# Kernel optimization log

Hardware: AMD Instinct MI355X
Metric: run time of the kernel (lower is better)

The kernel has to match this reference:

```python
import jax, jax.numpy as jnp
import numpy as np

D = 1024      # latent_dimension
NH = 8        # num_heads
ND = 256      # drug num_functions
NT = 128      # target num_functions
B = 128       # batch
EPS_LN = 1e-5
EPS_COS = 1e-8


def _proj_attend(x, W, b, in_w, in_b, out_w, out_b, g, beta):
    """ParallelFcWithAttention.forward: per-feature Linear(1,D)+ReLU, MHSA, LN, sum.
    x: (B, >=F); W,b: (F, D); in_w: (3D, D); out_w: (D, D); g,beta: (D,)."""
    F = W.shape[0]
    # fused batched scale+bias+ReLU replacing the Python loop of Linear(1,D)
    h = jax.nn.relu(x[:, :F, None] * W[None] + b[None])           # (B, F, D)
    Bsz = h.shape[0]
    qkv = h @ in_w.T + in_b                                       # (B, F, 3D)
    q, k, v = jnp.split(qkv, 3, axis=-1)
    Dh = D // NH
    def split_heads(t):
        return t.reshape(Bsz, F, NH, Dh).transpose(0, 2, 1, 3)   # (B, H, F, Dh)
    q, k, v = split_heads(q), split_heads(k), split_heads(v)
    scale = np.float32(1.0 / np.sqrt(Dh))
    scores = jnp.einsum('bhqd,bhkd->bhqk', q, k) * scale          # (B, H, F, F)
    attn = jax.nn.softmax(scores, axis=-1)
    o = jnp.einsum('bhqk,bhkd->bhqd', attn, v)                    # (B, H, F, Dh)
    o = o.transpose(0, 2, 1, 3).reshape(Bsz, F, D)
    o = o @ out_w.T + out_b
    mu = o.mean(axis=-1, keepdims=True)
    var = ((o - mu) ** 2).mean(axis=-1, keepdims=True)
    o = (o - mu) / jnp.sqrt(var + EPS_LN) * g + beta              # LayerNorm
    return o.sum(axis=1)                                          # (B, D)


def setup_inputs() -> dict:
    key = jax.random.key(0)
    ks = jax.random.split(key, 20)
    s = np.float32(0.02)
    inp = {
        'drug':    jax.random.normal(ks[0], (B, 2048), jnp.float32),
        'target':  jax.random.normal(ks[1], (B, 1024), jnp.float32),
        'dW':      jax.random.normal(ks[2], (ND, D), jnp.float32) * s,
        'db':      jax.random.normal(ks[3], (ND, D), jnp.float32) * s,
        'd_in_w':  jax.random.normal(ks[4], (3 * D, D), jnp.float32) * s,
        'd_in_b':  jnp.zeros((3 * D,), jnp.float32),
        'd_out_w': jax.random.normal(ks[5], (D, D), jnp.float32) * s,
        'd_out_b': jnp.zeros((D,), jnp.float32),
        'd_g':     jnp.ones((D,), jnp.float32),
        'd_beta':  jnp.zeros((D,), jnp.float32),
        'tW':      jax.random.normal(ks[6], (NT, D), jnp.float32) * s,
        'tb':      jax.random.normal(ks[7], (NT, D), jnp.float32) * s,
        't_in_w':  jax.random.normal(ks[8], (3 * D, D), jnp.float32) * s,
        't_in_b':  jnp.zeros((3 * D,), jnp.float32),
        't_out_w': jax.random.normal(ks[9], (D, D), jnp.float32) * s,
        't_out_b': jnp.zeros((D,), jnp.float32),
        't_g':     jnp.ones((D,), jnp.float32),
        't_beta':  jnp.zeros((D,), jnp.float32),
    }
    return inp


def reference(drug, target, dW, db, d_in_w, d_in_b, d_out_w, d_out_b, d_g, d_beta,
              tW, tb, t_in_w, t_in_b, t_out_w, t_out_b, t_g, t_beta):
    dp = _proj_attend(drug, dW, db, d_in_w, d_in_b, d_out_w, d_out_b, d_g, d_beta)   # (B, D)
    tp = _proj_attend(target, tW, tb, t_in_w, t_in_b, t_out_w, t_out_b, t_g, t_beta) # (B, D)
    # Cosine similarity over latent dim (torch CosineSimilarity dim=1), then sigmoid
    dot = jnp.sum(dp * tp, axis=-1)
    denom = jnp.maximum(jnp.linalg.norm(dp, axis=-1) * jnp.linalg.norm(tp, axis=-1), EPS_COS)
    return jax.nn.sigmoid(dot / denom)                                               # (B,)
```

## Files before the change

### kernel.cpp

```cpp
#include <hip/hip_runtime.h>

typedef unsigned short u16;
typedef unsigned int   u32;
typedef unsigned char  u8;

using bf16x8 = __attribute__((ext_vector_type(8))) short;
using f32x4  = __attribute__((ext_vector_type(4))) float;
using i32x4  = __attribute__((ext_vector_type(4))) int;

__device__ __forceinline__ float bf2f(u16 h) {
  u32 u = ((u32)h) << 16;
  return __builtin_bit_cast(float, u);
}
__device__ __forceinline__ u16 f2bf(float f) {
  u32 u = __builtin_bit_cast(u32, f);
  u += 0x7fffu + ((u >> 16) & 1u);
  return (u16)(u >> 16);
}

__device__ __forceinline__ void gload16(const void* src, void* ldsdst) {
  __builtin_amdgcn_global_load_lds(
      (const __attribute__((address_space(1))) void*)src,
      (__attribute__((address_space(3))) void*)ldsdst, 16, 0, 0);
}

__device__ __forceinline__ void mfma_i8(i32x4& c, i32x4 a, i32x4 b) {
  asm volatile("v_mfma_i32_16x16x64_i8 %0, %1, %2, %0" : "+a"(c) : "v"(a), "v"(b));
}

__device__ __forceinline__ int xcd_swz(int wg, int nwg) {
  int q = nwg >> 3, r = nwg & 7, xcd = wg & 7, loc = wg >> 3;
  return (xcd < r ? xcd * (q + 1) : r * (q + 1) + (xcd - r) * q) + loc;
}

__global__ __launch_bounds__(256) void cvt_w_i8(const float* __restrict__ in,
                                                u8* __restrict__ out,
                                                float* __restrict__ sc) {
  const int row  = blockIdx.x * 4 + (threadIdx.x >> 6);
  const int lane = threadIdx.x & 63;
  const float4* p = (const float4*)(in + (size_t)row * 1024 + lane * 16);
  float v[16];
  float mx = 0.f;
#pragma unroll
  for (int i = 0; i < 4; ++i) {
    float4 t = p[i];
    v[i * 4 + 0] = t.x; v[i * 4 + 1] = t.y; v[i * 4 + 2] = t.z; v[i * 4 + 3] = t.w;
#pragma unroll
    for (int j = 0; j < 4; ++j) mx = fmaxf(mx, fabsf(v[i * 4 + j]));
  }
#pragma unroll
  for (int m = 1; m < 64; m <<= 1) mx = fmaxf(mx, __shfl_xor(mx, m));
  const float scale = mx > 0.f ? 127.f / mx : 0.f;
  u32 pk[4];
#pragma unroll
  for (int i = 0; i < 4; ++i) {
    u32 b0 = (u32)(__float2int_rn(v[i * 4 + 0] * scale) & 0xff);
    u32 b1 = (u32)(__float2int_rn(v[i * 4 + 1] * scale) & 0xff);
    u32 b2 = (u32)(__float2int_rn(v[i * 4 + 2] * scale) & 0xff);
    u32 b3 = (u32)(__float2int_rn(v[i * 4 + 3] * scale) & 0xff);
    pk[i] = b0 | (b1 << 8) | (b2 << 16) | (b3 << 24);
  }
  *(uint4*)(out + (size_t)row * 1024 + lane * 16) = make_uint4(pk[0], pk[1], pk[2], pk[3]);
  if (lane == 0) sc[row] = mx > 0.f ? mx / 127.f : 0.f;
}

__global__ __launch_bounds__(256) void quant_i8(const u16* __restrict__ in,
                                                u8* __restrict__ out,
                                                float* __restrict__ sc) {
  const int row  = blockIdx.x * 4 + (threadIdx.x >> 6);
  const int lane = threadIdx.x & 63;
  const u16* p = in + (size_t)row * 1024 + lane * 16;
  float v[16];
  float mx = 0.f;
#pragma unroll
  for (int i = 0; i < 2; ++i) {
    bf16x8 t = *(const bf16x8*)(p + i * 8);
#pragma unroll
    for (int j = 0; j < 8; ++j) {
      float f = bf2f((u16)t[j]);
      v[i * 8 + j] = f;
      mx = fmaxf(mx, fabsf(f));
    }
  }
#pragma unroll
  for (int m = 1; m < 64; m <<= 1) mx = fmaxf(mx, __shfl_xor(mx, m));
  const float scale = mx > 0.f ? 127.f / mx : 0.f;
  u32 pk[4];
#pragma unroll
  for (int i = 0; i < 4; ++i) {
    u32 b0 = (u32)(__float2int_rn(v[i * 4 + 0] * scale) & 0xff);
    u32 b1 = (u32)(__float2int_rn(v[i * 4 + 1] * scale) & 0xff);
    u32 b2 = (u32)(__float2int_rn(v[i * 4 + 2] * scale) & 0xff);
    u32 b3 = (u32)(__float2int_rn(v[i * 4 + 3] * scale) & 0xff);
    pk[i] = b0 | (b1 << 8) | (b2 << 16) | (b3 << 24);
  }
  *(uint4*)(out + (size_t)row * 1024 + lane * 16) = make_uint4(pk[0], pk[1], pk[2], pk[3]);
  if (lane == 0) sc[row] = mx > 0.f ? mx / 127.f : 0.f;
}

__global__ __launch_bounds__(256) void hgen_i8(const float* __restrict__ x,
                                               const float* __restrict__ W,
                                               const float* __restrict__ bias,
                                               u8* __restrict__ h, float* __restrict__ hsc,
                                               int F, int logF, int b0, int xstride) {
  const int row  = blockIdx.x * 4 + (threadIdx.x >> 6);
  const int lane = threadIdx.x & 63;
  const int f = row & (F - 1);
  const int b = b0 + (row >> logF);
  const float xv = x[(size_t)b * xstride + f];
  const float4* wp = (const float4*)(W + (size_t)f * 1024 + lane * 16);
  const float4* bp = (const float4*)(bias + (size_t)f * 1024 + lane * 16);
  float hv[16];
  float mx = 0.f;
#pragma unroll
  for (int i = 0; i < 4; ++i) {
    float4 wv = wp[i];
    float4 bv = bp[i];
    hv[i * 4 + 0] = fmaxf(xv * wv.x + bv.x, 0.f);
    hv[i * 4 + 1] = fmaxf(xv * wv.y + bv.y, 0.f);
    hv[i * 4 + 2] = fmaxf(xv * wv.z + bv.z, 0.f);
    hv[i * 4 + 3] = fmaxf(xv * wv.w + bv.w, 0.f);
#pragma unroll
    for (int j = 0; j < 4; ++j) mx = fmaxf(mx, hv[i * 4 + j]);
  }
#pragma unroll
  for (int m = 1; m < 64; m <<= 1) mx = fmaxf(mx, __shfl_xor(mx, m));
  const float scale = mx > 0.f ? 127.f / mx : 0.f;
  u32 pk[4];
#pragma unroll
  for (int i = 0; i < 4; ++i) {
    u32 q0 = (u32)__float2int_rn(hv[i * 4 + 0] * scale);
    u32 q1 = (u32)__float2int_rn(hv[i * 4 + 1] * scale);
    u32 q2 = (u32)__float2int_rn(hv[i * 4 + 2] * scale);
    u32 q3 = (u32)__float2int_rn(hv[i * 4 + 3] * scale);
    pk[i] = q0 | (q1 << 8) | (q2 << 16) | (q3 << 24);
  }
  *(uint4*)(h + (size_t)row * 1024 + lane * 16) = make_uint4(pk[0], pk[1], pk[2], pk[3]);
  if (lane == 0) hsc[row] = mx > 0.f ? mx / 127.f : 0.f;
}

__global__ __launch_bounds__(512, 4) void gemm_i8(const u8* __restrict__ A,
                                                  const u8* __restrict__ B,
                                                  const float* __restrict__ sAsc,
                                                  const float* __restrict__ sBsc,
                                                  const float* __restrict__ bias,
                                                  u16* __restrict__ C,
                                                  int M, int N, int K) {
  __shared__ u8 sA[3][256 * 64];
  __shared__ u8 sB[3][128 * 64];
  const int tid  = threadIdx.x;
  const int lane = tid & 63;
  const int w    = tid >> 6;
  const int wm   = w >> 1;
  const int wn   = w & 1;

  const int nwg = gridDim.x * gridDim.y;
  const int wg  = blockIdx.y * gridDim.x + blockIdx.x;
  const int swz = xcd_swz(wg, nwg);
  const int n0 = (swz % gridDim.x) * 128;
  const int m0 = (swz / gridDim.x) * 256;

  i32x4 acc[4][4] = {};

  const int r_in  = lane >> 2;
  const int s_src = (lane & 3) ^ ((lane >> 3) & 3);

  auto stage = [&](int kt, int b) {
    const int k0 = kt << 6;
    gload16(A + (size_t)(m0 + w * 16 + r_in) * K + k0 + s_src * 16, &sA[b][w * 1024]);
    gload16(A + (size_t)(m0 + (w + 8) * 16 + r_in) * K + k0 + s_src * 16, &sA[b][(w + 8) * 1024]);
    gload16(B + (size_t)(n0 + w * 16 + r_in) * K + k0 + s_src * 16, &sB[b][w * 1024]);
  };

  const int NT = K >> 6;
  stage(0, 0);
  stage(1, 1);
  asm volatile("s_waitcnt vmcnt(3)" ::: "memory");
  __builtin_amdgcn_s_barrier();

  int cur = 0, nx = 2;
  for (int t = 0; t < NT; ++t) {
    const bool more = (t + 2 < NT);
    if (more) stage(t + 2, nx);

    i32x4 af[4], bg[4];
    const int g = lane >> 4;
#pragma unroll
    for (int mf = 0; mf < 4; ++mf) {
      int ra = wm * 64 + mf * 16 + (lane & 15);
      af[mf] = *(const i32x4*)(&sA[cur][ra * 64 + ((g ^ ((ra >> 1) & 3)) * 16)]);
    }
#pragma unroll
    for (int nf = 0; nf < 4; ++nf) {
      int rb = wn * 64 + nf * 16 + (lane & 15);
      bg[nf] = *(const i32x4*)(&sB[cur][rb * 64 + ((g ^ ((rb >> 1) & 3)) * 16)]);
    }
    asm volatile("s_waitcnt lgkmcnt(0)" ::: "memory");
    __builtin_amdgcn_sched_barrier(0);
    __builtin_amdgcn_s_setprio(1);
#pragma unroll
    for (int mf = 0; mf < 4; ++mf)
#pragma unroll
      for (int nf = 0; nf < 4; ++nf)
        mfma_i8(acc[mf][nf], af[mf], bg[nf]);
    __builtin_amdgcn_s_setprio(0);
    if (more) asm volatile("s_waitcnt vmcnt(3)" ::: "memory");
    else      asm volatile("s_waitcnt vmcnt(0)" ::: "memory");
    __builtin_amdgcn_s_barrier();
    cur = (cur == 2) ? 0 : cur + 1;
    nx  = (nx  == 2) ? 0 : nx  + 1;
  }

#pragma unroll
  for (int nf = 0; nf < 4; ++nf) {
    int cl = n0 + wn * 64 + nf * 16 + (lane & 15);
    float sb  = sBsc[cl];
    float bsv = bias[cl];
#pragma unroll
    for (int mf = 0; mf < 4; ++mf) {
      int r0 = m0 + wm * 64 + mf * 16 + (lane >> 4) * 4;
      float4 sa4 = *(const float4*)(sAsc + r0);
      const float* sap = (const float*)&sa4;
#pragma unroll
      for (int reg = 0; reg < 4; ++reg)
        C[(size_t)(r0 + reg) * N + cl] =
            f2bf((float)acc[mf][nf][reg] * (sap[reg] * sb) + bsv);
    }
  }
}

__global__ __launch_bounds__(512, 4) void attn(const u16* __restrict__ qkv,
                                               u16* __restrict__ o_out, int F) {
  __shared__ u16 k_lds[64 * 136];
  __shared__ u16 vT[128 * 72];
  __shared__ u16 p_lds[8 * 16 * 72];

  const int tid  = threadIdx.x;
  const int lane = tid & 63;
  const int w    = tid >> 6;

  const int swzb = xcd_swz(blockIdx.x, gridDim.x);
  const int nqb  = F >> 7;
  const int qb   = swzb % nqb;
  const int head = (swzb / nqb) & 7;
  const int bc   = swzb / (nqb * 8);

  const size_t rowbase = (size_t)bc * F * 3072;
  const float scale = 0.08838834764831845f;

  const int qr = lane & 15;
  const int g4 = lane >> 4;

  bf16x8 qreg[4];
  {
    const u16* qsrc = qkv + rowbase +
                      (size_t)(qb * 128 + w * 16 + qr) * 3072 + head * 128;
#pragma unroll
    for (int kk = 0; kk < 4; ++kk) {
      bf16x8 v = *(const bf16x8*)(qsrc + kk * 32 + 8 * g4);
#pragma unroll
      for (int j = 0; j < 8; ++j) v[j] = (short)f2bf(bf2f((u16)v[j]) * scale);
      qreg[kk] = v;
    }
  }

  f32x4 o_acc[8] = {};
  float m_run = -INFINITY, l_run = 0.f;

  const int nkb = F >> 6;
  for (int kb = 0; kb < nkb; ++kb) {
    __syncthreads();
    const u16* ksrc = qkv + rowbase + (size_t)(kb * 64) * 3072 + 1024 + head * 128;
    const u16* vsrc = ksrc + 1024;
    for (int it = tid; it < 1024; it += 512) {
      int r = it >> 4, s = it & 15;
      *(bf16x8*)(k_lds + r * 136 + s * 8) = *(const bf16x8*)(ksrc + (size_t)r * 3072 + s * 8);
    }
    {
      int g2 = tid >> 4, s = tid & 15;
      const u16* v0 = vsrc + (size_t)(2 * g2) * 3072 + s * 8;
      bf16x8 a = *(const bf16x8*)(v0);
      bf16x8 b = *(const bf16x8*)(v0 + 3072);
      int rs0 = (2 * g2) ^ ((s & 7) << 3);
      int d0  = s * 8;
#pragma unroll
      for (int j = 0; j < 8; ++j) {
        u32 pk = (u32)(u16)a[j] | ((u32)(u16)b[j] << 16);
        *(u32*)(vT + (d0 + j) * 72 + rs0) = pk;
      }
    }
    __syncthreads();

    f32x4 sa[4] = {};
#pragma unroll
    for (int kk = 0; kk < 4; ++kk) {
#pragma unroll
      for (int f = 0; f < 4; ++f) {
        bf16x8 ak = *(const bf16x8*)(k_lds + (f * 16 + qr) * 136 + kk * 32 + 8 * g4);
        sa[f] = __builtin_amdgcn_mfma_f32_16x16x32_bf16(ak, qreg[kk], sa[f], 0, 0, 0);
      }
    }

    float tmax = -INFINITY;
#pragma unroll
    for (int f = 0; f < 4; ++f)
#pragma unroll
      for (int rr = 0; rr < 4; ++rr) tmax = fmaxf(tmax, sa[f][rr]);
    tmax = fmaxf(tmax, __shfl_xor(tmax, 16));
    tmax = fmaxf(tmax, __shfl_xor(tmax, 32));
    float mnew  = fmaxf(m_run, tmax);
    float alpha = __expf(m_run - mnew);
    float psum  = 0.f;
#pragma unroll
    for (int f = 0; f < 4; ++f) {
      u16 pp[4];
#pragma unroll
      for (int rr = 0; rr < 4; ++rr) {
        float p = __expf(sa[f][rr] - mnew);
        psum += p;
        pp[rr] = f2bf(p);
      }
      uint2 u;
      u.x = (u32)pp[0] | ((u32)pp[1] << 16);
      u.y = (u32)pp[2] | ((u32)pp[3] << 16);
      *(uint2*)(p_lds + w * 1152 + qr * 72 + f * 16 + g4 * 4) = u;
    }
    psum += __shfl_xor(psum, 16);
    psum += __shfl_xor(psum, 32);
    l_run = l_run * alpha + psum;
    m_run = mnew;

#pragma unroll
    for (int rr = 0; rr < 4; ++rr) {
      float ar = __shfl(alpha, g4 * 4 + rr);
#pragma unroll
      for (int g = 0; g < 8; ++g) o_acc[g][rr] *= ar;
    }

#pragma unroll
    for (int kk2 = 0; kk2 < 2; ++kk2) {
      bf16x8 pa = *(const bf16x8*)(p_lds + w * 1152 + qr * 72 + kk2 * 32 + 8 * g4);
#pragma unroll
      for (int g = 0; g < 8; ++g) {
        int swv = ((g * 2 + (qr >> 3)) & 7) << 3;
        bf16x8 vb = *(const bf16x8*)(vT + (g * 16 + qr) * 72 + ((kk2 * 32 + 8 * g4) ^ swv));
        o_acc[g] = __builtin_amdgcn_mfma_f32_16x16x32_bf16(pa, vb, o_acc[g], 0, 0, 0);
      }
    }
  }

  float linv = 1.f / l_run;
#pragma unroll
  for (int rr = 0; rr < 4; ++rr) {
    float lr = __shfl(linv, g4 * 4 + rr);
    size_t row = (size_t)bc * F + qb * 128 + w * 16 + g4 * 4 + rr;
#pragma unroll
    for (int g = 0; g < 8; ++g)
      o_out[row * 1024 + head * 128 + g * 16 + qr] = f2bf(o_acc[g][rr] * lr);
  }
}

__global__ __launch_bounds__(256) void ln_stats(const u16* __restrict__ proj,
                                                float2* __restrict__ stats) {
  int row  = blockIdx.x * 4 + (threadIdx.x >> 6);
  int lane = threadIdx.x & 63;
  const u16* p = proj + (size_t)row * 1024;
  float s = 0.f, s2 = 0.f;
#pragma unroll
  for (int i = 0; i < 2; ++i) {
    bf16x8 v = *(const bf16x8*)(p + (lane + i * 64) * 8);
#pragma unroll
    for (int j = 0; j < 8; ++j) { float f = bf2f((u16)v[j]); s += f; s2 += f * f; }
  }
#pragma unroll
  for (int m = 1; m < 64; m <<= 1) { s += __shfl_xor(s, m); s2 += __shfl_xor(s2, m); }
  if (lane == 0) {
    float mu  = s * (1.f / 1024.f);
    float var = s2 * (1.f / 1024.f) - mu * mu;
    stats[row] = make_float2(mu, rsqrtf(var + 1e-5f));
  }
}

__global__ __launch_bounds__(256) void ln_accum(const u16* __restrict__ proj,
                                                const float2* __restrict__ stats,
                                                const float* __restrict__ g,
                                                const float* __restrict__ beta,
                                                float* __restrict__ dp, int F, int b0) {
  int d  = blockIdx.x * 256 + threadIdx.x;
  int bc = blockIdx.z;
  int f0 = blockIdx.y * 64;
  const u16* base = proj + ((size_t)(bc * F + f0)) * 1024 + d;
  const float2* st = stats + bc * F + f0;
  float acc = 0.f;
  for (int f = 0; f < 64; ++f) {
    float2 s = st[f];
    acc += (bf2f(base[(size_t)f * 1024]) - s.x) * s.y;
  }
  acc = acc * g[d] + 64.f * beta[d];
  atomicAdd(&dp[(size_t)(b0 + bc) * 1024 + d], acc);
}

__global__ __launch_bounds__(256) void cosine_sig(const float* __restrict__ dp,
                                                  const float* __restrict__ tp,
                                                  float* __restrict__ out) {
  __shared__ float red[3][4];
  int b = blockIdx.x;
  int tid = threadIdx.x, lane = tid & 63, w = tid >> 6;
  float dot = 0.f, n1 = 0.f, n2 = 0.f;
  for (int i = tid; i < 1024; i += 256) {
    float a = dp[(size_t)b * 1024 + i], c = tp[(size_t)b * 1024 + i];
    dot += a * c; n1 += a * a; n2 += c * c;
  }
#pragma unroll
  for (int m = 1; m < 64; m <<= 1) {
    dot += __shfl_xor(dot, m); n1 += __shfl_xor(n1, m); n2 += __shfl_xor(n2, m);
  }
  if (lane == 0) { red[0][w] = dot; red[1][w] = n1; red[2][w] = n2; }
  __syncthreads();
  if (tid == 0) {
    dot = red[0][0] + red[0][1] + red[0][2] + red[0][3];
    n1  = red[1][0] + red[1][1] + red[1][2] + red[1][3];
    n2  = red[2][0] + red[2][1] + red[2][2] + red[2][3];
    float denom = fmaxf(sqrtf(n1) * sqrtf(n2), 1e-8f);
    out[b] = 1.f / (1.f + __expf(-dot / denom));
  }
}

extern "C" void kernel_launch(void* const* d_in, const int* in_sizes, int n_in,
                              void* d_out, int out_size, void* d_ws, size_t ws_size,
                              hipStream_t stream) {
  const float* drug   = (const float*)d_in[0];
  const float* target = (const float*)d_in[1];

  char* p = (char*)d_ws;
  auto alloc = [&](size_t bytes) -> char* {
    char* r = p; p += (bytes + 255) & ~(size_t)255; return r;
  };

  u8*    w8_d    = (u8*)alloc((size_t)3072 * 1024);
  float* wsc_d   = (float*)alloc((size_t)3072 * 4);
  u8*    w8_t    = (u8*)alloc((size_t)3072 * 1024);
  float* wsc_t   = (float*)alloc((size_t)3072 * 4);
  u8*    w8o_d   = (u8*)alloc((size_t)1024 * 1024);
  float* wsco_d  = (float*)alloc((size_t)1024 * 4);
  u8*    w8o_t   = (u8*)alloc((size_t)1024 * 1024);
  float* wsco_t  = (float*)alloc((size_t)1024 * 4);
  float* dp      = (float*)alloc((size_t)2 * 128 * 1024 * 4);
  float* tp      = dp + 128 * 1024;

  size_t fixed = (size_t)(p - (char*)d_ws);
  size_t per = (size_t)256 * 1024
             + (size_t)256 * 4
             + (size_t)256 * 3072 * 2
             + (size_t)256 * 1024 * 2 * 2
             + (size_t)256 * 8 + 4096;
  int Bc = 8;
  if      (fixed + 128 * per <= ws_size) Bc = 128;
  else if (fixed +  64 * per <= ws_size) Bc = 64;
  else if (fixed +  32 * per <= ws_size) Bc = 32;
  else if (fixed +  16 * per <= ws_size) Bc = 16;

  u8*    h8     = (u8*)alloc((size_t)Bc * 256 * 1024);
  float* hsc    = (float*)alloc((size_t)Bc * 256 * 4);
  u16*   qkvbuf = (u16*)alloc((size_t)Bc * 256 * 3072 * 2);
  u16*   obuf   = (u16*)alloc((size_t)Bc * 256 * 1024 * 2);
  u16*   projbuf= (u16*)alloc((size_t)Bc * 256 * 1024 * 2);
  float2* statsb = (float2*)alloc((size_t)Bc * 256 * 8);

  cvt_w_i8<<<768, 256, 0, stream>>>((const float*)d_in[4],  w8_d, wsc_d);
  cvt_w_i8<<<768, 256, 0, stream>>>((const float*)d_in[12], w8_t, wsc_t);
  cvt_w_i8<<<256, 256, 0, stream>>>((const float*)d_in[6],  w8o_d, wsco_d);
  cvt_w_i8<<<256, 256, 0, stream>>>((const float*)d_in[14], w8o_t, wsco_t);
  hipMemsetAsync(dp, 0, (size_t)2 * 128 * 1024 * 4, stream);

  for (int br = 0; br < 2; ++br) {
    const int F = br ? 128 : 256, logF = br ? 7 : 8, xstride = br ? 1024 : 2048;
    const float* x    = br ? target : drug;
    const float* W    = (const float*)d_in[br ? 10 : 2];
    const float* Wb   = (const float*)d_in[br ? 11 : 3];
    u8*          w8   = br ? w8_t : w8_d;
    float*       wsc  = br ? wsc_t : wsc_d;
    const float* inb  = (const float*)d_in[br ? 13 : 5];
    u8*          w8o  = br ? w8o_t : w8o_d;
    float*       wsco = br ? wsco_t : wsco_d;
    const float* outb = (const float*)d_in[br ? 15 : 7];
    const float* gg   = (const float*)d_in[br ? 16 : 8];
    const float* bb   = (const float*)d_in[br ? 17 : 9];
    float*       accp = br ? tp : dp;

    const int nb = (br ? (2 * Bc > 128 ? 128 : 2 * Bc) : (Bc > 128 ? 128 : Bc));

    for (int b0 = 0; b0 < 128; b0 += nb) {
      const int Mr = nb * F;
      hgen_i8<<<Mr / 4, 256, 0, stream>>>(x, W, Wb, h8, hsc, F, logF, b0, xstride);
      gemm_i8<<<dim3(3072 / 128, Mr / 256), 512, 0, stream>>>(h8, w8, hsc, wsc, inb, qkvbuf, Mr, 3072, 1024);
      attn<<<(F / 128) * 8 * nb, 512, 0, stream>>>(qkvbuf, obuf, F);
      quant_i8<<<Mr / 4, 256, 0, stream>>>(obuf, h8, hsc);
      gemm_i8<<<dim3(1024 / 128, Mr / 256), 512, 0, stream>>>(h8, w8o, hsc, wsco, outb, projbuf, Mr, 1024, 1024);
      ln_stats<<<Mr / 4, 256, 0, stream>>>(projbuf, statsb);
      ln_accum<<<dim3(4, F / 64, nb), 256, 0, stream>>>(projbuf, statsb, gg, bb, accp, F, b0);
    }
  }
  cosine_sig<<<128, 256, 0, stream>>>(dp, tp, (float*)d_out);
}
```

Measured before the change: 579.7 us.

## Fuse LayerNorm stats into out-proj GEMM epilogue; restructure attention block per head

The out-projection GEMM epilogue now accumulates per-row sum and sum-of-squares and adds them into a zeroed stats buffer with atomics. A tiny finalize kernel replaces the separate ln_stats pass, so the projection no longer has to be re-read. Attention now launches one block per (batch, head) with F/16 waves, so K/V tiles are loaded once per head instead of once per 128-query block. Softmax switches to exp2 with the log2e factor folded into the Q scale, and rescaling is skipped unless the max grows by more than 8. Costs are atomic contention, an extra memset, and large blocks that limit occupancy for F=256.

```diff
diff --git a/kernel.cpp b/kernel.cpp
--- a/kernel.cpp
+++ b/kernel.cpp
@@ -139,12 +139,14 @@
   if (lane == 0) hsc[row] = mx > 0.f ? mx / 127.f : 0.f;
 }
 
+template <bool STATS>
 __global__ __launch_bounds__(512, 4) void gemm_i8(const u8* __restrict__ A,
                                                   const u8* __restrict__ B,
                                                   const float* __restrict__ sAsc,
                                                   const float* __restrict__ sBsc,
                                                   const float* __restrict__ bias,
                                                   u16* __restrict__ C,
+                                                  float2* __restrict__ stats,
                                                   int M, int N, int K) {
   __shared__ u8 sA[3][256 * 64];
   __shared__ u8 sB[3][128 * 64];
@@ -211,50 +213,72 @@
     nx  = (nx  == 2) ? 0 : nx  + 1;
   }
 
+  float sb4[4], bs4[4];
 #pragma unroll
   for (int nf = 0; nf < 4; ++nf) {
     int cl = n0 + wn * 64 + nf * 16 + (lane & 15);
-    float sb  = sBsc[cl];
-    float bsv = bias[cl];
-#pragma unroll
-    for (int mf = 0; mf < 4; ++mf) {
-      int r0 = m0 + wm * 64 + mf * 16 + (lane >> 4) * 4;
-      float4 sa4 = *(const float4*)(sAsc + r0);
-      const float* sap = (const float*)&sa4;
-#pragma unroll
-      for (int reg = 0; reg < 4; ++reg)
-        C[(size_t)(r0 + reg) * N + cl] =
-            f2bf((float)acc[mf][nf][reg] * (sap[reg] * sb) + bsv);
-    }
-  }
-}
-
-__global__ __launch_bounds__(512, 4) void attn(const u16* __restrict__ qkv,
-                                               u16* __restrict__ o_out, int F) {
+    sb4[nf] = sBsc[cl];
+    bs4[nf] = bias[cl];
+  }
+#pragma unroll
+  for (int mf = 0; mf < 4; ++mf) {
+    int r0 = m0 + wm * 64 + mf * 16 + (lane >> 4) * 4;
+    float4 sa4 = *(const float4*)(sAsc + r0);
+    const float* sap = (const float*)&sa4;
+#pragma unroll
+    for (int reg = 0; reg < 4; ++reg) {
+      float s = 0.f, s2 = 0.f;
+#pragma unroll
+      for (int nf = 0; nf < 4; ++nf) {
+        int cl = n0 + wn * 64 + nf * 16 + (lane & 15);
+        float v = (float)acc[mf][nf][reg] * (sap[reg] * sb4[nf]) + bs4[nf];
+        C[(size_t)(r0 + reg) * N + cl] = f2bf(v);
+        if (STATS) { s += v; s2 += v * v; }
+      }
+      if (STATS) {
+#pragma unroll
+        for (int m = 1; m < 16; m <<= 1) { s += __shfl_xor(s, m); s2 += __shfl_xor(s2, m); }
+        if ((lane & 15) == 0) {
+          atomicAdd(&stats[r0 + reg].x, s);
+          atomicAdd(&stats[r0 + reg].y, s2);
+        }
+      }
+    }
+  }
+}
+
+__global__ __launch_bounds__(256) void ln_fin(float2* __restrict__ stats, int n) {
+  int i = blockIdx.x * 256 + threadIdx.x;
+  if (i >= n) return;
+  float2 s = stats[i];
+  float mu  = s.x * (1.f / 1024.f);
+  float var = s.y * (1.f / 1024.f) - mu * mu;
+  stats[i] = make_float2(mu, rsqrtf(var + 1e-5f));
+}
+
+__global__ __launch_bounds__(1024) void attn(const u16* __restrict__ qkv,
+                                             u16* __restrict__ o_out, int F) {
   __shared__ u16 k_lds[64 * 136];
   __shared__ u16 vT[128 * 72];
-  __shared__ u16 p_lds[8 * 16 * 72];
+  __shared__ u16 p_lds[16 * 16 * 72];
 
   const int tid  = threadIdx.x;
   const int lane = tid & 63;
   const int w    = tid >> 6;
-
-  const int swzb = xcd_swz(blockIdx.x, gridDim.x);
-  const int nqb  = F >> 7;
-  const int qb   = swzb % nqb;
-  const int head = (swzb / nqb) & 7;
-  const int bc   = swzb / (nqb * 8);
+  const int nt   = blockDim.x;
+
+  const int head = blockIdx.x & 7;
+  const int bc   = blockIdx.x >> 3;
 
   const size_t rowbase = (size_t)bc * F * 3072;
-  const float scale = 0.08838834764831845f;
+  const float scale = 0.12751744865678818f;
 
   const int qr = lane & 15;
   const int g4 = lane >> 4;
 
   bf16x8 qreg[4];
   {
-    const u16* qsrc = qkv + rowbase +
-                      (size_t)(qb * 128 + w * 16 + qr) * 3072 + head * 128;
+    const u16* qsrc = qkv + rowbase + (size_t)(w * 16 + qr) * 3072 + head * 128;
 #pragma unroll
     for (int kk = 0; kk < 4; ++kk) {
       bf16x8 v = *(const bf16x8*)(qsrc + kk * 32 + 8 * g4);
@@ -272,12 +296,12 @@
     __syncthreads();
     const u16* ksrc = qkv + rowbase + (size_t)(kb * 64) * 3072 + 1024 + head * 128;
     const u16* vsrc = ksrc + 1024;
-    for (int it = tid; it < 1024; it += 512) {
+    for (int it = tid; it < 1024; it += nt) {
       int r = it >> 4, s = it & 15;
       *(bf16x8*)(k_lds + r * 136 + s * 8) = *(const bf16x8*)(ksrc + (size_t)r * 3072 + s * 8);
     }
-    {
-      int g2 = tid >> 4, s = tid & 15;
+    for (int it = tid; it < 512; it += nt) {
+      int g2 = it >> 4, s = it & 15;
       const u16* v0 = vsrc + (size_t)(2 * g2) * 3072 + s * 8;
       bf16x8 a = *(const bf16x8*)(v0);
       bf16x8 b = *(const bf16x8*)(v0 + 3072);
@@ -308,15 +332,18 @@
       for (int rr = 0; rr < 4; ++rr) tmax = fmaxf(tmax, sa[f][rr]);
     tmax = fmaxf(tmax, __shfl_xor(tmax, 16));
     tmax = fmaxf(tmax, __shfl_xor(tmax, 32));
-    float mnew  = fmaxf(m_run, tmax);
-    float alpha = __expf(m_run - mnew);
-    float psum  = 0.f;
+
+    const bool ns = !__all(tmax - m_run <= 8.f);
+    float mnew = m_run, alpha = 1.f;
+    if (ns) { mnew = fmaxf(m_run, tmax); alpha = exp2f(m_run - mnew); }
+
+    float psum = 0.f;
 #pragma unroll
     for (int f = 0; f < 4; ++f) {
       u16 pp[4];
 #pragma unroll
       for (int rr = 0; rr < 4; ++rr) {
-        float p = __expf(sa[f][rr] - mnew);
+        float p = exp2f(sa[f][rr] - mnew);
         psum += p;
         pp[rr] = f2bf(p);
       }
@@ -330,11 +357,13 @@
     l_run = l_run * alpha + psum;
     m_run = mnew;
 
-#pragma unroll
-    for (int rr = 0; rr < 4; ++rr) {
-      float ar = __shfl(alpha, g4 * 4 + rr);
-#pragma unroll
-      for (int g = 0; g < 8; ++g) o_acc[g][rr] *= ar;
+    if (ns) {
+#pragma unroll
+      for (int rr = 0; rr < 4; ++rr) {
+        float ar = __shfl(alpha, g4 * 4 + rr);
+#pragma unroll
+        for (int g = 0; g < 8; ++g) o_acc[g][rr] *= ar;
+      }
     }
 
 #pragma unroll
@@ -353,31 +382,10 @@
 #pragma unroll
   for (int rr = 0; rr < 4; ++rr) {
     float lr = __shfl(linv, g4 * 4 + rr);
-    size_t row = (size_t)bc * F + qb * 128 + w * 16 + g4 * 4 + rr;
+    size_t row = (size_t)bc * F + w * 16 + g4 * 4 + rr;
 #pragma unroll
     for (int g = 0; g < 8; ++g)
       o_out[row * 1024 + head * 128 + g * 16 + qr] = f2bf(o_acc[g][rr] * lr);
-  }
-}
-
-__global__ __launch_bounds__(256) void ln_stats(const u16* __restrict__ proj,
-                                                float2* __restrict__ stats) {
-  int row  = blockIdx.x * 4 + (threadIdx.x >> 6);
-  int lane = threadIdx.x & 63;
-  const u16* p = proj + (size_t)row * 1024;
-  float s = 0.f, s2 = 0.f;
-#pragma unroll
-  for (int i = 0; i < 2; ++i) {
-    bf16x8 v = *(const bf16x8*)(p + (lane + i * 64) * 8);
-#pragma unroll
-    for (int j = 0; j < 8; ++j) { float f = bf2f((u16)v[j]); s += f; s2 += f * f; }
-  }
-#pragma unroll
-  for (int m = 1; m < 64; m <<= 1) { s += __shfl_xor(s, m); s2 += __shfl_xor(s2, m); }
-  if (lane == 0) {
-    float mu  = s * (1.f / 1024.f);
-    float var = s2 * (1.f / 1024.f) - mu * mu;
-    stats[row] = make_float2(mu, rsqrtf(var + 1e-5f));
   }
 }
 
@@ -493,11 +501,14 @@
     for (int b0 = 0; b0 < 128; b0 += nb) {
       const int Mr = nb * F;
       hgen_i8<<<Mr / 4, 256, 0, stream>>>(x, W, Wb, h8, hsc, F, logF, b0, xstride);
-      gemm_i8<<<dim3(3072 / 128, Mr / 256), 512, 0, stream>>>(h8, w8, hsc, wsc, inb, qkvbuf, Mr, 3072, 1024);
-      attn<<<(F / 128) * 8 * nb, 512, 0, stream>>>(qkvbuf, obuf, F);
+      gemm_i8<false><<<dim3(3072 / 128, Mr / 256), 512, 0, stream>>>(
+          h8, w8, hsc, wsc, inb, qkvbuf, nullptr, Mr, 3072, 1024);
+      attn<<<8 * nb, 64 * (F / 16), 0, stream>>>(qkvbuf, obuf, F);
       quant_i8<<<Mr / 4, 256, 0, stream>>>(obuf, h8, hsc);
-      gemm_i8<<<dim3(1024 / 128, Mr / 256), 512, 0, stream>>>(h8, w8o, hsc, wsco, outb, projbuf, Mr, 1024, 1024);
-      ln_stats<<<Mr / 4, 256, 0, stream>>>(projbuf, statsb);
+      hipMemsetAsync(statsb, 0, (size_t)Mr * 8, stream);
+      gemm_i8<true><<<dim3(1024 / 128, Mr / 256), 512, 0, stream>>>(
+          h8, w8o, hsc, wsco, outb, projbuf, statsb, Mr, 1024, 1024);
+      ln_fin<<<(Mr + 255) / 256, 256, 0, stream>>>(statsb, Mr);
       ln_accum<<<dim3(4, F / 64, nb), 256, 0, stream>>>(projbuf, statsb, gg, bb, accp, F, b0);
     }
   }
```

Result: faster. 532.1 us (-8.2%).
